# Optimization experiments

Measured on AMD Instinct MI355X. Metric: run time of the kernel, lower is better.

Reference implementation:

```python
import jax, jax.numpy as jnp
import numpy as np

DIM = 3072
NUM_HEADS = 24
HEAD_DIM = DIM // NUM_HEADS  # 128
EPS = 1e-6


def rms_norm(x, scale):
    # x: (..., D); torch F.rms_norm over last dim
    var = jnp.mean(jnp.square(x), axis=-1, keepdims=True)
    return x * jax.lax.rsqrt(var + EPS) * scale


def apply_rope(xq, xk, freqs_cis):
    # xq, xk: (B, H, L, D); freqs_cis: (1, 1, L, D//2, 2, 2)
    B, H, L, D = xq.shape
    xq_ = xq.astype(jnp.float32).reshape(B, H, L, D // 2, 1, 2)
    xk_ = xk.astype(jnp.float32).reshape(B, H, L, D // 2, 1, 2)
    # (1,1,L,D/2,2) * (B,H,L,D/2,1) broadcast -> (B,H,L,D/2,2)
    xq_out = freqs_cis[..., 0] * xq_[..., 0] + freqs_cis[..., 1] * xq_[..., 1]
    xk_out = freqs_cis[..., 0] * xk_[..., 0] + freqs_cis[..., 1] * xk_[..., 1]
    return xq_out.reshape(B, H, L, D).astype(xq.dtype), xk_out.reshape(B, H, L, D).astype(xk.dtype)


def setup_inputs() -> dict:
    key = jax.random.key(0)
    ks = jax.random.split(key, 7)
    B, L = 1, 2048
    x = jax.random.normal(ks[0], (B, L, DIM), dtype=jnp.float32)
    pe = jax.random.normal(ks[1], (1, 1, L, HEAD_DIM // 2, 2, 2), dtype=jnp.float32)
    # parameters (torch nn.Linear layout: weight is (out, in))
    s = 1.0 / np.sqrt(DIM)
    w_qkv = jax.random.uniform(ks[2], (3 * DIM, DIM), minval=-s, maxval=s, dtype=jnp.float32)
    w_proj = jax.random.uniform(ks[3], (DIM, DIM), minval=-s, maxval=s, dtype=jnp.float32)
    b_proj = jax.random.uniform(ks[4], (DIM,), minval=-s, maxval=s, dtype=jnp.float32)
    q_scale = jnp.ones((HEAD_DIM,), dtype=jnp.float32)
    k_scale = jnp.ones((HEAD_DIM,), dtype=jnp.float32)
    return {"x": x, "pe": pe, "w_qkv": w_qkv, "w_proj": w_proj,
            "b_proj": b_proj, "q_scale": q_scale, "k_scale": k_scale}


def reference(x, pe, w_qkv, w_proj, b_proj, q_scale, k_scale):
    B, L, _ = x.shape
    qkv = x @ w_qkv.T  # (B, L, 3*DIM)
    qkv = qkv.reshape(B, L, 3, NUM_HEADS, HEAD_DIM)
    qkv = jnp.transpose(qkv, (2, 0, 3, 1, 4))  # (3, B, H, L, D)
    q, k, v = qkv[0], qkv[1], qkv[2]
    # QKNorm (RMSNorm over head_dim)
    q = rms_norm(q, q_scale)
    k = rms_norm(k, k_scale)
    # RoPE
    q, k = apply_rope(q, k, pe)
    # SDPA: softmax(q k^T / sqrt(D)) v, non-causal
    scores = jnp.einsum("bhqd,bhkd->bhqk", q, k) / np.sqrt(HEAD_DIM).astype(np.float32)
    attn = jax.nn.softmax(scores, axis=-1)
    out = jnp.einsum("bhqk,bhkd->bhqd", attn, v)  # (B, H, L, D)
    out = jnp.transpose(out, (0, 2, 1, 3)).reshape(B, L, DIM)  # B L (H D)
    return out @ w_proj.T + b_proj
```

## Files before the change

kernel.cpp:

```cpp
#include <hip/hip_runtime.h>
#include <hip/hip_bf16.h>

typedef _Float16 f16;
typedef _Float16 f16x2 __attribute__((ext_vector_type(2)));
typedef _Float16 f16x4 __attribute__((ext_vector_type(4)));
typedef _Float16 f16x8 __attribute__((ext_vector_type(8)));
typedef float f32x4 __attribute__((ext_vector_type(4)));

#define L_SEQ 2048
#define DIM 3072
#define NHEAD 24
#define HDIM 128

__device__ __forceinline__ void gll16(const f16* g, f16* l) {
    __builtin_amdgcn_global_load_lds((const __attribute__((address_space(1))) void*)g,
                                     (__attribute__((address_space(3))) void*)l, 16, 0, 0);
}

__global__ __launch_bounds__(256) void cvt3_kernel(const float* __restrict__ s0, f16* __restrict__ d0, int n0,
                                                   const float* __restrict__ s1, f16* __restrict__ d1, int n1,
                                                   const float* __restrict__ s2, f16* __restrict__ d2, int n2) {
    int i = blockIdx.x * blockDim.x + threadIdx.x;
    int stride = gridDim.x * blockDim.x;
    for (int j = i; j < n0; j += stride) {
        float4 v = reinterpret_cast<const float4*>(s0)[j];
        f16x4 o = {(f16)v.x, (f16)v.y, (f16)v.z, (f16)v.w};
        reinterpret_cast<f16x4*>(d0)[j] = o;
    }
    for (int j = i; j < n1; j += stride) {
        float4 v = reinterpret_cast<const float4*>(s1)[j];
        f16x4 o = {(f16)v.x, (f16)v.y, (f16)v.z, (f16)v.w};
        reinterpret_cast<f16x4*>(d1)[j] = o;
    }
    for (int j = i; j < n2; j += stride) {
        float4 v = reinterpret_cast<const float4*>(s2)[j];
        f16x4 o = {(f16)v.x, (f16)v.y, (f16)v.z, (f16)v.w};
        reinterpret_cast<f16x4*>(d2)[j] = o;
    }
}

#define GEMM_BODY_S(T, VM, DO_STAGE)                                                    \
    {                                                                                   \
        asm volatile("s_waitcnt vmcnt(" #VM ")" ::: "memory");                          \
        __builtin_amdgcn_s_barrier();                                                   \
        __builtin_amdgcn_sched_barrier(0);                                              \
        const int slot_ = (T) % 3;                                                      \
        f16x8 af[4], bf[4];                                                             \
        _Pragma("unroll") for (int i = 0; i < 4; i++)                                   \
            af[i] = *reinterpret_cast<const f16x8*>(                                    \
                &As[slot_][(wr + i * 16 + laneM) * 32 + fc16]);                         \
        _Pragma("unroll") for (int j = 0; j < 4; j++)                                   \
            bf[j] = *reinterpret_cast<const f16x8*>(                                    \
                &Bs[slot_][(wc + j * 16 + laneM) * 32 + fc16]);                         \
        if (DO_STAGE) {                                                                 \
            const int t2 = (T) + 2;                                                     \
            const int s2 = t2 % 3;                                                      \
            gll16(Asrc + t2 * 32, &As[s2][dstoff]);                                     \
            gll16(Asrc + (size_t)64 * K + t2 * 32, &As[s2][2048 + dstoff]);             \
            gll16(Bsrc + t2 * 32, &Bs[s2][dstoff]);                                     \
            gll16(Bsrc + (size_t)64 * K + t2 * 32, &Bs[s2][2048 + dstoff]);             \
        }                                                                               \
        __builtin_amdgcn_s_setprio(1);                                                  \
        _Pragma("unroll") for (int i = 0; i < 4; i++)                                   \
            _Pragma("unroll") for (int j = 0; j < 4; j++)                               \
                acc[i][j] =                                                             \
                    __builtin_amdgcn_mfma_f32_16x16x32_f16(af[i], bf[j], acc[i][j],     \
                                                           0, 0, 0);                    \
        __builtin_amdgcn_s_setprio(0);                                                  \
    }

template <int MODE>
__global__ __launch_bounds__(256, 4) void rg128_gemm(const f16* __restrict__ A,
                                                     const f16* __restrict__ B,
                                                     f16* __restrict__ Cf16,
                                                     f16* __restrict__ vT,
                                                     float* __restrict__ Cf32,
                                                     const float* __restrict__ bias,
                                                     int M, int N, int K) {
    __shared__ f16 As[3][128 * 32];
    __shared__ f16 Bs[3][128 * 32];
    const int tid = threadIdx.x;
    const int wid = tid >> 6;
    const int lane = tid & 63;
    const int grp = lane >> 4;
    const int laneM = lane & 15;

    const int nwg = gridDim.x * gridDim.y;
    const int orig = blockIdx.y * gridDim.x + blockIdx.x;
    const int wgid = (orig & 7) * (nwg >> 3) + (orig >> 3);
    const int by = wgid % gridDim.y;
    const int bx = wgid / gridDim.y;
    const int m0 = by * 128;
    const int n0 = bx * 128;

    const int wr = (wid >> 1) * 64;
    const int wc = (wid & 1) * 64;
    const int NT = K >> 5;
    const int fc16 = (grp ^ ((laneM >> 1) & 3)) * 8;

    const int srow = tid >> 2;
    const int scol = (((tid & 3) ^ ((tid >> 3) & 3)) << 3);
    const f16* Asrc = A + (size_t)(m0 + srow) * K + scol;
    const f16* Bsrc = B + (size_t)(n0 + srow) * K + scol;
    const int dstoff = wid * 512;

    const f32x4 vzero = {0.f, 0.f, 0.f, 0.f};
    f32x4 acc[4][4];
#pragma unroll
    for (int i = 0; i < 4; i++)
#pragma unroll
        for (int j = 0; j < 4; j++) acc[i][j] = vzero;

#pragma unroll
    for (int t = 0; t < 2; t++) {
        gll16(Asrc + t * 32, &As[t][dstoff]);
        gll16(Asrc + (size_t)64 * K + t * 32, &As[t][2048 + dstoff]);
        gll16(Bsrc + t * 32, &Bs[t][dstoff]);
        gll16(Bsrc + (size_t)64 * K + t * 32, &Bs[t][2048 + dstoff]);
    }

    int t = 0;
    for (; t < NT - 2; ++t) GEMM_BODY_S(t, 4, true);
    GEMM_BODY_S(t, 4, false); ++t;
    GEMM_BODY_S(t, 0, false);

    if (MODE == 1) {
#pragma unroll
        for (int i = 0; i < 4; i++)
#pragma unroll
            for (int j = 0; j < 4; j++)
#pragma unroll
                for (int r = 0; r < 4; r++) {
                    int row = m0 + wr + i * 16 + grp * 4 + r;
                    int col = n0 + wc + j * 16 + laneM;
                    Cf32[(size_t)row * N + col] = acc[i][j][r] + bias[col];
                }
    } else if (n0 < 2 * DIM) {
#pragma unroll
        for (int i = 0; i < 4; i++)
#pragma unroll
            for (int j = 0; j < 4; j++)
#pragma unroll
                for (int r = 0; r < 4; r++) {
                    int row = m0 + wr + i * 16 + grp * 4 + r;
                    int col = n0 + wc + j * 16 + laneM;
                    Cf16[(size_t)row * N + col] = (f16)acc[i][j][r];
                }
    } else {
#pragma unroll
        for (int i = 0; i < 4; i++)
#pragma unroll
            for (int j = 0; j < 4; j++) {
                int hd = n0 - 2 * DIM + wc + j * 16 + laneM;
                int row0 = m0 + wr + i * 16 + grp * 4;
                f16x4 pk;
#pragma unroll
                for (int r = 0; r < 4; r++) pk[r] = (f16)acc[i][j][r];
                *reinterpret_cast<f16x4*>(&vT[(size_t)hd * L_SEQ + row0]) = pk;
            }
    }
}

__global__ __launch_bounds__(256) void fuse_qk_kernel(const f16* __restrict__ qkv,
                                                      const float* __restrict__ pe,
                                                      const float* __restrict__ qs,
                                                      const float* __restrict__ ks,
                                                      f16* __restrict__ qb,
                                                      f16* __restrict__ kb) {
    const int l = blockIdx.x;
    const int h = blockIdx.y * 4 + (threadIdx.x >> 6);
    const int i = threadIdx.x & 63;
    const f16* row = qkv + (size_t)l * (3 * DIM) + h * HDIM;
    f16x2 qp = *reinterpret_cast<const f16x2*>(row + 2 * i);
    f16x2 kp = *reinterpret_cast<const f16x2*>(row + DIM + 2 * i);
    float q0 = (float)qp[0], q1 = (float)qp[1];
    float k0 = (float)kp[0], k1 = (float)kp[1];
    float sq = q0 * q0 + q1 * q1;
    float sk = k0 * k0 + k1 * k1;
#pragma unroll
    for (int off = 1; off < 64; off <<= 1) {
        sq += __shfl_xor(sq, off);
        sk += __shfl_xor(sk, off);
    }
    const float SCALE = 0.08838834764831845f;
    float rq = rsqrtf(sq * (1.0f / 128.0f) + 1e-6f) * SCALE;
    float rk = rsqrtf(sk * (1.0f / 128.0f) + 1e-6f);
    float4 w = *reinterpret_cast<const float4*>(pe + ((size_t)l * 64 + i) * 4);
    float qa = q0 * rq * qs[2 * i];
    float qbv = q1 * rq * qs[2 * i + 1];
    float ka = k0 * rk * ks[2 * i];
    float kbv = k1 * rk * ks[2 * i + 1];
    f16x2 qo = {(f16)(w.x * qa + w.y * qbv), (f16)(w.z * qa + w.w * qbv)};
    f16x2 ko = {(f16)(w.x * ka + w.y * kbv), (f16)(w.z * ka + w.w * kbv)};
    *reinterpret_cast<f16x2*>(qb + ((size_t)h * L_SEQ + l) * HDIM + 2 * i) = qo;
    *reinterpret_cast<f16x2*>(kb + ((size_t)h * L_SEQ + l) * HDIM + 2 * i) = ko;
}

#define KVBLK 64
#define NSTEP (L_SEQ / KVBLK)

__device__ __forceinline__ void stage_kv(const f16* __restrict__ Kh,
                                         const f16* __restrict__ Vh,
                                         int k0, f16* Kt, f16* Vt, int tid) {
    const int wid = tid >> 6;
    const int krow = tid >> 4;
    const int kcl = (tid & 15) ^ (krow & 7);
    const int vrow = tid >> 3;
    const int vcl = (tid & 7) ^ (vrow & 7);
#pragma unroll
    for (int i = 0; i < 4; i++)
        gll16(Kh + (size_t)(k0 + i * 16 + krow) * HDIM + kcl * 8, Kt + i * 2048 + wid * 512);
#pragma unroll
    for (int i = 0; i < 4; i++)
        gll16(Vh + (size_t)(i * 32 + vrow) * L_SEQ + k0 + vcl * 8, Vt + i * 2048 + wid * 512);
}

__global__ __launch_bounds__(256, 2) void attn_kernel(const f16* __restrict__ qb,
                                                      const f16* __restrict__ kb,
                                                      const f16* __restrict__ vT,
                                                      f16* __restrict__ attnb) {
    __shared__ f16 Kt[2][64 * 128];
    __shared__ f16 Vt[2][128 * 64];
    __shared__ f16 Pl[4][16 * 72];
    const int tid = threadIdx.x;
    const int wid = tid >> 6;
    const int lane = tid & 63;
    const int grp = lane >> 4;
    const int laneM = lane & 15;

    const int nwg = gridDim.x * gridDim.y;
    const int orig = blockIdx.y * gridDim.x + blockIdx.x;
    const int wgid = (orig & 7) * (nwg >> 3) + (orig >> 3);
    const int h = wgid / gridDim.x;
    const int q0 = (wgid % gridDim.x) * 128 + wid * 32;

    const f16* Qh = qb + (size_t)h * L_SEQ * HDIM;
    const f16* Kh = kb + (size_t)h * L_SEQ * HDIM;
    const f16* Vh = vT + (size_t)h * HDIM * L_SEQ;

    f16x8 qf[2][4];
#pragma unroll
    for (int g = 0; g < 2; g++)
#pragma unroll
        for (int c = 0; c < 4; c++)
            qf[g][c] = *reinterpret_cast<const f16x8*>(
                Qh + (size_t)(q0 + g * 16 + laneM) * HDIM + c * 32 + grp * 8);

    const f32x4 vzero = {0.f, 0.f, 0.f, 0.f};
    f32x4 O[2][8];
#pragma unroll
    for (int g = 0; g < 2; g++)
#pragma unroll
        for (int f = 0; f < 8; f++) O[g][f] = vzero;
    float m[2] = {-3.0e38f, -3.0e38f};
    float lsum[2] = {0.f, 0.f};
    f16* Prow = &Pl[wid][laneM * 72];
    const int swz = laneM & 7;

    stage_kv(Kh, Vh, 0, Kt[0], Vt[0], tid);

    for (int step = 0; step < NSTEP; ++step) {
        const int cur = step & 1;
        __syncthreads();
        if (step + 1 < NSTEP)
            stage_kv(Kh, Vh, (step + 1) * KVBLK, Kt[cur ^ 1], Vt[cur ^ 1], tid);
        const f16* Kc = Kt[cur];
        const f16* Vc = Vt[cur];

        f32x4 s[2][4];
#pragma unroll
        for (int g = 0; g < 2; g++)
#pragma unroll
            for (int cc = 0; cc < 4; cc++) s[g][cc] = vzero;
#pragma unroll
        for (int cc = 0; cc < 4; cc++) {
            f16x8 kf[4];
#pragma unroll
            for (int c = 0; c < 4; c++)
                kf[c] = *reinterpret_cast<const f16x8*>(
                    &Kc[(cc * 16 + laneM) * 128 + (((c * 4 + grp) ^ swz) * 8)]);
#pragma unroll
            for (int c = 0; c < 4; c++) {
                s[0][cc] = __builtin_amdgcn_mfma_f32_16x16x32_f16(kf[c], qf[0][c], s[0][cc], 0, 0, 0);
                s[1][cc] = __builtin_amdgcn_mfma_f32_16x16x32_f16(kf[c], qf[1][c], s[1][cc], 0, 0, 0);
            }
        }

#pragma unroll
        for (int g = 0; g < 2; g++) {
            float pmax = s[g][0][0];
#pragma unroll
            for (int cc = 0; cc < 4; cc++)
#pragma unroll
                for (int r = 0; r < 4; r++) pmax = fmaxf(pmax, s[g][cc][r]);
            if (!__all(pmax <= m[g] + 8.0f)) {
                float pm = fmaxf(pmax, __shfl_xor(pmax, 16));
                pm = fmaxf(pm, __shfl_xor(pm, 32));
                float mnew = fmaxf(m[g], pm);
                float alpha = __expf(m[g] - mnew);
                m[g] = mnew;
                lsum[g] *= alpha;
                float af[4];
#pragma unroll
                for (int r = 0; r < 4; r++) af[r] = __shfl(alpha, grp * 4 + r);
#pragma unroll
                for (int f = 0; f < 8; f++)
#pragma unroll
                    for (int r = 0; r < 4; r++) O[g][f][r] *= af[r];
            }
            float ps = 0.f;
#pragma unroll
            for (int cc = 0; cc < 4; cc++) {
                f16x4 pk;
#pragma unroll
                for (int r = 0; r < 4; r++) {
                    float p = __expf(s[g][cc][r] - m[g]);
                    ps += p;
                    pk[r] = (f16)p;
                }
                *reinterpret_cast<f16x4*>(Prow + cc * 16 + grp * 4) = pk;
            }
            ps += __shfl_xor(ps, 16);
            ps += __shfl_xor(ps, 32);
            lsum[g] += ps;

#pragma unroll
            for (int z = 0; z < 2; z++) {
                f16x8 pa = *reinterpret_cast<const f16x8*>(Prow + z * 32 + grp * 8);
#pragma unroll
                for (int f = 0; f < 8; f++) {
                    f16x8 vf = *reinterpret_cast<const f16x8*>(
                        &Vc[(f * 16 + laneM) * 64 + (((z * 4 + grp) ^ swz) * 8)]);
                    O[g][f] = __builtin_amdgcn_mfma_f32_16x16x32_f16(pa, vf, O[g][f], 0, 0, 0);
                }
            }
        }
    }

#pragma unroll
    for (int g = 0; g < 2; g++) {
        float li = 1.0f / lsum[g];
        float lf[4];
#pragma unroll
        for (int r = 0; r < 4; r++) lf[r] = __shfl(li, grp * 4 + r);
#pragma unroll
        for (int f = 0; f < 8; f++)
#pragma unroll
            for (int r = 0; r < 4; r++) {
                int row = q0 + g * 16 + grp * 4 + r;
                attnb[(size_t)row * DIM + h * HDIM + f * 16 + laneM] = (f16)(O[g][f][r] * lf[r]);
            }
    }
}

extern "C" void kernel_launch(void* const* d_in, const int* in_sizes, int n_in,
                              void* d_out, int out_size, void* d_ws, size_t ws_size,
                              hipStream_t stream) {
    const float* x = (const float*)d_in[0];
    const float* pe = (const float*)d_in[1];
    const float* w_qkv = (const float*)d_in[2];
    const float* w_proj = (const float*)d_in[3];
    const float* b_proj = (const float*)d_in[4];
    const float* q_scale = (const float*)d_in[5];
    const float* k_scale = (const float*)d_in[6];
    float* out = (float*)d_out;

    char* ws = (char*)d_ws;
    f16* xb     = (f16*)(ws + 0);
    f16* wqkvb  = (f16*)(ws + 12582912);
    f16* wprojb = (f16*)(ws + 69206016);
    f16* qkvb   = (f16*)(ws + 88080384);
    f16* qbuf   = (f16*)(ws + 125829120);
    f16* kbuf   = (f16*)(ws + 138412032);
    f16* vT     = (f16*)(ws + 150994944);
    f16* attnb  = (f16*)(ws + 163577856);
    if (ws_size < 176160768) return;

    cvt3_kernel<<<2048, 256, 0, stream>>>(x, xb, (2048 * 3072) / 4,
                                          w_qkv, wqkvb, (9216 * 3072) / 4,
                                          w_proj, wprojb, (3072 * 3072) / 4);

    rg128_gemm<0><<<dim3(72, 16), 256, 0, stream>>>(xb, wqkvb, qkvb, vT, nullptr, nullptr,
                                                    2048, 9216, 3072);
    fuse_qk_kernel<<<dim3(2048, 6), 256, 0, stream>>>(qkvb, pe, q_scale, k_scale, qbuf, kbuf);
    attn_kernel<<<dim3(16, 24), 256, 0, stream>>>(qbuf, kbuf, vT, attnb);
    rg128_gemm<1><<<dim3(24, 16), 256, 0, stream>>>(attnb, wprojb, nullptr, nullptr, out, b_proj,
                                                    2048, 3072, 3072);
}
```

Baseline: 341.3 us.

## Use 256x128 tiles with 512-thread blocks for the QKV GEMM

Adds a dedicated QKV GEMM kernel with 256-row M tiles and 8 waves per block, so each B tile staged in LDS is shared across twice as many output rows. The grid halves to 72x8 blocks and each thread now issues three async loads per k-step instead of four. The projection GEMM becomes its own non-templated kernel with unchanged behaviour. Larger blocks use more LDS and registers per block, which lowers the number of resident blocks per CU, and fewer blocks in the grid can worsen wave-quantization across CUs.

```diff
diff --git a/kernel.cpp b/kernel.cpp
--- a/kernel.cpp
+++ b/kernel.cpp
@@ -36,6 +36,113 @@
         float4 v = reinterpret_cast<const float4*>(s2)[j];
         f16x4 o = {(f16)v.x, (f16)v.y, (f16)v.z, (f16)v.w};
         reinterpret_cast<f16x4*>(d2)[j] = o;
+    }
+}
+
+#define GEMM_BODY_L(T, VM, DO_STAGE)                                                    \
+    {                                                                                   \
+        asm volatile("s_waitcnt vmcnt(" #VM ")" ::: "memory");                          \
+        __builtin_amdgcn_s_barrier();                                                   \
+        __builtin_amdgcn_sched_barrier(0);                                              \
+        const int slot_ = (T) % 3;                                                      \
+        f16x8 af[4], bf[4];                                                             \
+        _Pragma("unroll") for (int i = 0; i < 4; i++)                                   \
+            af[i] = *reinterpret_cast<const f16x8*>(                                    \
+                &As[slot_][(wr + i * 16 + laneM) * 32 + fc16]);                         \
+        _Pragma("unroll") for (int j = 0; j < 4; j++)                                   \
+            bf[j] = *reinterpret_cast<const f16x8*>(                                    \
+                &Bs[slot_][(wc + j * 16 + laneM) * 32 + fc16]);                         \
+        if (DO_STAGE) {                                                                 \
+            const int t2 = (T) + 2;                                                     \
+            const int s2 = t2 % 3;                                                      \
+            gll16(Asrc0 + t2 * 32, &As[s2][dstoff]);                                    \
+            gll16(Asrc1 + t2 * 32, &As[s2][4096 + dstoff]);                             \
+            gll16(Bsrc + t2 * 32, &Bs[s2][dstoff]);                                     \
+        }                                                                               \
+        __builtin_amdgcn_s_setprio(1);                                                  \
+        _Pragma("unroll") for (int i = 0; i < 4; i++)                                   \
+            _Pragma("unroll") for (int j = 0; j < 4; j++)                               \
+                acc[i][j] =                                                             \
+                    __builtin_amdgcn_mfma_f32_16x16x32_f16(af[i], bf[j], acc[i][j],     \
+                                                           0, 0, 0);                    \
+        __builtin_amdgcn_s_setprio(0);                                                  \
+    }
+
+__global__ __launch_bounds__(512, 4) void qkv_gemm(const f16* __restrict__ A,
+                                                   const f16* __restrict__ B,
+                                                   f16* __restrict__ Cf16,
+                                                   f16* __restrict__ vT,
+                                                   int M, int N, int K) {
+    __shared__ f16 As[3][256 * 32];
+    __shared__ f16 Bs[3][128 * 32];
+    const int tid = threadIdx.x;
+    const int wid = tid >> 6;
+    const int lane = tid & 63;
+    const int grp = lane >> 4;
+    const int laneM = lane & 15;
+
+    const int nwg = gridDim.x * gridDim.y;
+    const int orig = blockIdx.y * gridDim.x + blockIdx.x;
+    const int wgid = (orig & 7) * (nwg >> 3) + (orig >> 3);
+    const int by = wgid % gridDim.y;
+    const int bx = wgid / gridDim.y;
+    const int m0 = by * 256;
+    const int n0 = bx * 128;
+
+    const int wr = (wid >> 1) * 64;
+    const int wc = (wid & 1) * 64;
+    const int NT = K >> 5;
+    const int fc16 = (grp ^ ((laneM >> 1) & 3)) * 8;
+
+    const int srow = tid >> 2;
+    const int scol = (((tid & 3) ^ ((tid >> 3) & 3)) << 3);
+    const f16* Asrc0 = A + (size_t)(m0 + srow) * K + scol;
+    const f16* Asrc1 = A + (size_t)(m0 + 128 + srow) * K + scol;
+    const f16* Bsrc = B + (size_t)(n0 + srow) * K + scol;
+    const int dstoff = wid * 512;
+
+    const f32x4 vzero = {0.f, 0.f, 0.f, 0.f};
+    f32x4 acc[4][4];
+#pragma unroll
+    for (int i = 0; i < 4; i++)
+#pragma unroll
+        for (int j = 0; j < 4; j++) acc[i][j] = vzero;
+
+#pragma unroll
+    for (int t = 0; t < 2; t++) {
+        gll16(Asrc0 + t * 32, &As[t][dstoff]);
+        gll16(Asrc1 + t * 32, &As[t][4096 + dstoff]);
+        gll16(Bsrc + t * 32, &Bs[t][dstoff]);
+    }
+
+    int t = 0;
+    for (; t < NT - 2; ++t) GEMM_BODY_L(t, 3, true);
+    GEMM_BODY_L(t, 3, false); ++t;
+    GEMM_BODY_L(t, 0, false);
+
+    if (n0 < 2 * DIM) {
+#pragma unroll
+        for (int i = 0; i < 4; i++)
+#pragma unroll
+            for (int j = 0; j < 4; j++)
+#pragma unroll
+                for (int r = 0; r < 4; r++) {
+                    int row = m0 + wr + i * 16 + grp * 4 + r;
+                    int col = n0 + wc + j * 16 + laneM;
+                    Cf16[(size_t)row * N + col] = (f16)acc[i][j][r];
+                }
+    } else {
+#pragma unroll
+        for (int i = 0; i < 4; i++)
+#pragma unroll
+            for (int j = 0; j < 4; j++) {
+                int hd = n0 - 2 * DIM + wc + j * 16 + laneM;
+                int row0 = m0 + wr + i * 16 + grp * 4;
+                f16x4 pk;
+#pragma unroll
+                for (int r = 0; r < 4; r++) pk[r] = (f16)acc[i][j][r];
+                *reinterpret_cast<f16x4*>(&vT[(size_t)hd * L_SEQ + row0]) = pk;
+            }
     }
 }
 
@@ -69,14 +176,11 @@
         __builtin_amdgcn_s_setprio(0);                                                  \
     }
 
-template <int MODE>
-__global__ __launch_bounds__(256, 4) void rg128_gemm(const f16* __restrict__ A,
-                                                     const f16* __restrict__ B,
-                                                     f16* __restrict__ Cf16,
-                                                     f16* __restrict__ vT,
-                                                     float* __restrict__ Cf32,
-                                                     const float* __restrict__ bias,
-                                                     int M, int N, int K) {
+__global__ __launch_bounds__(256, 4) void proj_gemm(const f16* __restrict__ A,
+                                                    const f16* __restrict__ B,
+                                                    float* __restrict__ Cf32,
+                                                    const float* __restrict__ bias,
+                                                    int M, int N, int K) {
     __shared__ f16 As[3][128 * 32];
     __shared__ f16 Bs[3][128 * 32];
     const int tid = threadIdx.x;
@@ -124,41 +228,16 @@
     GEMM_BODY_S(t, 4, false); ++t;
     GEMM_BODY_S(t, 0, false);
 
-    if (MODE == 1) {
-#pragma unroll
-        for (int i = 0; i < 4; i++)
-#pragma unroll
-            for (int j = 0; j < 4; j++)
-#pragma unroll
-                for (int r = 0; r < 4; r++) {
-                    int row = m0 + wr + i * 16 + grp * 4 + r;
-                    int col = n0 + wc + j * 16 + laneM;
-                    Cf32[(size_t)row * N + col] = acc[i][j][r] + bias[col];
-                }
-    } else if (n0 < 2 * DIM) {
-#pragma unroll
-        for (int i = 0; i < 4; i++)
-#pragma unroll
-            for (int j = 0; j < 4; j++)
-#pragma unroll
-                for (int r = 0; r < 4; r++) {
-                    int row = m0 + wr + i * 16 + grp * 4 + r;
-                    int col = n0 + wc + j * 16 + laneM;
-                    Cf16[(size_t)row * N + col] = (f16)acc[i][j][r];
-                }
-    } else {
-#pragma unroll
-        for (int i = 0; i < 4; i++)
-#pragma unroll
-            for (int j = 0; j < 4; j++) {
-                int hd = n0 - 2 * DIM + wc + j * 16 + laneM;
-                int row0 = m0 + wr + i * 16 + grp * 4;
-                f16x4 pk;
-#pragma unroll
-                for (int r = 0; r < 4; r++) pk[r] = (f16)acc[i][j][r];
-                *reinterpret_cast<f16x4*>(&vT[(size_t)hd * L_SEQ + row0]) = pk;
-            }
-    }
+#pragma unroll
+    for (int i = 0; i < 4; i++)
+#pragma unroll
+        for (int j = 0; j < 4; j++)
+#pragma unroll
+            for (int r = 0; r < 4; r++) {
+                int row = m0 + wr + i * 16 + grp * 4 + r;
+                int col = n0 + wc + j * 16 + laneM;
+                Cf32[(size_t)row * N + col] = acc[i][j][r] + bias[col];
+            }
 }
 
 __global__ __launch_bounds__(256) void fuse_qk_kernel(const f16* __restrict__ qkv,
@@ -380,10 +459,9 @@
                                           w_qkv, wqkvb, (9216 * 3072) / 4,
                                           w_proj, wprojb, (3072 * 3072) / 4);
 
-    rg128_gemm<0><<<dim3(72, 16), 256, 0, stream>>>(xb, wqkvb, qkvb, vT, nullptr, nullptr,
-                                                    2048, 9216, 3072);
+    qkv_gemm<<<dim3(72, 8), 512, 0, stream>>>(xb, wqkvb, qkvb, vT, 2048, 9216, 3072);
     fuse_qk_kernel<<<dim3(2048, 6), 256, 0, stream>>>(qkvb, pe, q_scale, k_scale, qbuf, kbuf);
     attn_kernel<<<dim3(16, 24), 256, 0, stream>>>(qbuf, kbuf, vT, attnb);
-    rg128_gemm<1><<<dim3(24, 16), 256, 0, stream>>>(attnb, wprojb, nullptr, nullptr, out, b_proj,
-                                                    2048, 3072, 3072);
-}
+    proj_gemm<<<dim3(24, 16), 256, 0, stream>>>(attnb, wprojb, out, b_proj,
+                                                2048, 3072, 3072);
+}
```

After: 353.7 us. 3.6% more time.
